# Performance work log

Measured on AMD Instinct MI355X. Metric: run time of the kernel, lower is better.

Reference implementation:

```python
import jax, jax.numpy as jnp
import numpy as np

SIGMA = 0.15
POS_W, ANG_W, WID_W, SCORE_W = 1.0, 1.0, 1.0, 0.5


def setup_inputs() -> dict:
    N, MAXC = 262144, 32
    rng = np.random.default_rng(0)
    counts = rng.integers(0, MAXC, size=N)
    M = int(counts.sum())
    key = jax.random.key(0)
    k1, k2, k3 = jax.random.split(key, 3)
    pred = jax.random.normal(k1, (N, 6), jnp.float32)
    gt = jax.random.normal(k2, (M, 6), jnp.float32)
    # GT score is a BCE target: keep it in [0, 1)
    gt = gt.at[:, 5].set(jax.random.uniform(k3, (M,), jnp.float32))
    return {
        "pred": pred,
        "all_gt_grasps": gt,
        "gt_counts": jnp.asarray(counts, jnp.int32),
    }


def reference(pred, all_gt_grasps, gt_counts):
    N = pred.shape[0]
    M = all_gt_grasps.shape[0]
    # CSR-style ragged layout: segment id of each GT row
    seg = jnp.repeat(jnp.arange(N), gt_counts, total_repeat_length=M)  # (M,)
    has_gt = gt_counts > 0                                             # (N,)

    # Step 1: squared distance from each GT to its prediction's center
    ppos = pred[seg, :2]                                               # (M,2)
    sq_dist = jnp.sum((ppos - all_gt_grasps[:, :2]) ** 2, axis=1)      # (M,)

    # Step 2: Gaussian tolerance position loss (per-segment max response)
    resp = jnp.exp(-sq_dist / (2.0 * SIGMA ** 2))
    max_resp = jax.ops.segment_max(resp, seg, num_segments=N)
    loss_pos = jnp.where(has_gt, 1.0 - max_resp, 0.0)

    # Step 3: nearest GT per prediction (first argmin, matching torch.argmin)
    seg_min = jax.ops.segment_min(sq_dist, seg, num_segments=N)
    cand = jnp.where(sq_dist == seg_min[seg], jnp.arange(M), M)
    nearest = jax.ops.segment_min(cand, seg, num_segments=N)
    nearest = jnp.where(has_gt, jnp.minimum(nearest, M - 1), 0)
    ng = all_gt_grasps[nearest]                                        # (N,6)

    # Step 4: angle (L1 on cos/sin), width (smooth L1), score (BCE-with-logits)
    loss_angle = jnp.where(
        has_gt,
        jnp.abs(pred[:, 2] - ng[:, 2]) + jnp.abs(pred[:, 3] - ng[:, 3]),
        0.0,
    )
    d = pred[:, 4] - ng[:, 4]
    ad = jnp.abs(d)
    smooth_l1 = jnp.where(ad < 1.0, 0.5 * d * d, ad - 0.5)
    loss_width = jnp.where(has_gt, smooth_l1, 0.0)

    x, t = pred[:, 5], ng[:, 5]
    bce = jnp.maximum(x, 0.0) - x * t + jnp.log1p(jnp.exp(-jnp.abs(x)))
    loss_score = jnp.where(has_gt & (t > 0), bce, 0.0)

    lp = loss_pos.mean()
    la = loss_angle.mean()
    lw = loss_width.mean()
    ls = loss_score.mean()
    lg = POS_W * lp + ANG_W * la + WID_W * lw + SCORE_W * ls
    return jnp.stack([lp, la, lw, ls, lg])
```

## Files before the change

kernel.cpp:

```cpp
#include <hip/hip_runtime.h>
#include <math.h>
#include <float.h>

#define BS 256
#define MAXC 31
typedef unsigned int u32;


__global__ void block_sum_kernel(const int* __restrict__ counts,
                                 int* __restrict__ blockSums, int N) {
    int i = blockIdx.x * BS + threadIdx.x;
    int v = (i < N) ? counts[i] : 0;
    for (int o = 32; o > 0; o >>= 1) v += __shfl_down(v, o, 64);
    __shared__ int ws[BS / 64];
    int lane = threadIdx.x & 63, w = threadIdx.x >> 6;
    if (lane == 0) ws[w] = v;
    __syncthreads();
    if (threadIdx.x == 0) {
        int s = 0;
        for (int ww = 0; ww < BS / 64; ++ww) s += ws[ww];
        blockSums[blockIdx.x] = s;
    }
}

__global__ void __launch_bounds__(BS)
fused_kernel(const float* __restrict__ pred, const float* __restrict__ gt,
             const int* __restrict__ counts, const int* __restrict__ blockSums,
             float4* __restrict__ partials, int N) {
    const int t = threadIdx.x;
    const int b = blockIdx.x;
    const int i = b * BS + t;
    const int lane = t & 63, w = t >> 6;

    __shared__ int waveTot[BS / 64];
    __shared__ int basePart[BS / 64];
    __shared__ float red[BS / 64][4];

    const int c = (i < N) ? counts[i] : 0;
    int incl = c;
    for (int o = 1; o < 64; o <<= 1) {
        int x = __shfl_up(incl, o, 64);
        if (lane >= o) incl += x;
    }
    if (lane == 63) waveTot[w] = incl;

    int acc = 0;
#pragma unroll
    for (int k = 0; k < 4; ++k) {
        const int idx = t + BS * k;
        if (idx < b) acc += blockSums[idx];
    }
    for (int o = 32; o > 0; o >>= 1) acc += __shfl_down(acc, o, 64);
    if (lane == 0) basePart[w] = acc;
    __syncthreads();

    int wbase = 0;
    for (int ww = 0; ww < w; ++ww) wbase += waveTot[ww];
    const int base = basePart[0] + basePart[1] + basePart[2] + basePart[3];
    const int gStart = base + wbase + incl - c;

    const float2* gxy = reinterpret_cast<const float2*>(gt);
    const float2 myp = (i < N)
        ? reinterpret_cast<const float2*>(pred)[(size_t)i * 3]
        : make_float2(0.f, 0.f);

    float best = FLT_MAX;
    int bestRow = 0;

#pragma unroll
    for (int j = 0; j < MAXC; ++j) {
        if (j < c) {
            const float2 g = gxy[(size_t)(gStart + j) * 3];
            const float dx = myp.x - g.x, dy = myp.y - g.y;
            const float d2 = dx * dx + dy * dy;
            if (d2 < best) { best = d2; bestRow = gStart + j; }
        }
    }

    float lp = 0.f, la = 0.f, lw = 0.f, ls = 0.f;
    if (i < N && c > 0) {
        lp = 1.0f - expf(-best / 0.045f);

        const float* p = pred + (size_t)i * 6;
        const float2 p23 = *reinterpret_cast<const float2*>(p + 2);
        const float2 p45 = *reinterpret_cast<const float2*>(p + 4);
        const float* ng = gt + (size_t)bestRow * 6;
        const float2 g23 = *reinterpret_cast<const float2*>(ng + 2);
        const float2 g45 = *reinterpret_cast<const float2*>(ng + 4);

        la = fabsf(p23.x - g23.x) + fabsf(p23.y - g23.y);
        const float d = p45.x - g45.x;
        const float ad = fabsf(d);
        lw = (ad < 1.0f) ? 0.5f * d * d : ad - 0.5f;
        const float x = p45.y;
        if (g45.y > 0.0f) {
            ls = fmaxf(x, 0.0f) - x * g45.y + log1pf(expf(-fabsf(x)));
        }
    }

    for (int o = 32; o > 0; o >>= 1) {
        lp += __shfl_down(lp, o, 64);
        la += __shfl_down(la, o, 64);
        lw += __shfl_down(lw, o, 64);
        ls += __shfl_down(ls, o, 64);
    }
    if (lane == 0) { red[w][0] = lp; red[w][1] = la; red[w][2] = lw; red[w][3] = ls; }
    __syncthreads();
    if (t == 0) {
        float s0 = 0, s1 = 0, s2 = 0, s3 = 0;
        for (int ww = 0; ww < BS / 64; ++ww) {
            s0 += red[ww][0]; s1 += red[ww][1]; s2 += red[ww][2]; s3 += red[ww][3];
        }
        partials[b] = make_float4(s0, s1, s2, s3);
    }
}

__global__ void finalize_kernel(const float4* __restrict__ partials,
                                float* __restrict__ out, int nb, int N) {
    const int t = threadIdx.x;
    const int lane = t & 63, w = t >> 6;
    double s0 = 0, s1 = 0, s2 = 0, s3 = 0;
    if (t < nb) {
        const float4 v = partials[t];
        s0 = v.x; s1 = v.y; s2 = v.z; s3 = v.w;
    }
    for (int o = 32; o > 0; o >>= 1) {
        s0 += __shfl_down(s0, o, 64);
        s1 += __shfl_down(s1, o, 64);
        s2 += __shfl_down(s2, o, 64);
        s3 += __shfl_down(s3, o, 64);
    }
    __shared__ double red[16][4];
    if (lane == 0) { red[w][0] = s0; red[w][1] = s1; red[w][2] = s2; red[w][3] = s3; }
    __syncthreads();
    if (t == 0) {
        double t0 = 0, t1 = 0, t2 = 0, t3 = 0;
        for (int ww = 0; ww < blockDim.x / 64; ++ww) {
            t0 += red[ww][0]; t1 += red[ww][1]; t2 += red[ww][2]; t3 += red[ww][3];
        }
        const double inv = 1.0 / (double)N;
        const float lp = (float)(t0 * inv);
        const float la = (float)(t1 * inv);
        const float lw = (float)(t2 * inv);
        const float ls = (float)(t3 * inv);
        out[0] = lp; out[1] = la; out[2] = lw; out[3] = ls;
        out[4] = lp + la + lw + 0.5f * ls;
    }
}

extern "C" void kernel_launch(void* const* d_in, const int* in_sizes, int n_in,
                              void* d_out, int out_size, void* d_ws, size_t ws_size,
                              hipStream_t stream) {
    const float* pred = (const float*)d_in[0];
    const float* gt = (const float*)d_in[1];
    const int* counts = (const int*)d_in[2];
    float* out = (float*)d_out;

    const int N = in_sizes[2];
    const int numBlocks = (N + BS - 1) / BS;

    int* blockSums = (int*)d_ws;
    float4* partials = (float4*)((char*)d_ws + 8192);

    block_sum_kernel<<<numBlocks, BS, 0, stream>>>(counts, blockSums, N);
    fused_kernel<<<numBlocks, BS, 0, stream>>>(pred, gt, counts, blockSums,
                                               partials, N);
    finalize_kernel<<<1, 1024, 0, stream>>>(partials, out, numBlocks, N);
}
```

Baseline: 179.7 us.

## Stage block's GT rows in shared memory via coalesced float4 loads

Each block now cooperatively copies its contiguous range of GT rows into LDS in chunks of 1536 rows, using coalesced float4 loads aligned via a pad row. Threads then scan their own segment from shared memory and keep the nearest GT's angle, width and score fields in registers, which removes the strided per-thread gathers and the second global load of the nearest row. The cost is about 36KB of LDS per block, which lowers occupancy, plus extra barriers and a chunk loop.

```diff
diff --git a/kernel.cpp b/kernel.cpp
--- a/kernel.cpp
+++ b/kernel.cpp
@@ -4,7 +4,9 @@
 
 #define BS 256
 #define MAXC 31
-typedef unsigned int u32;
+#define CH 1536
+#define CHF4 (CH * 24 / 16)
+#define LPT (CHF4 / BS)
 
 
 __global__ void block_sum_kernel(const int* __restrict__ counts,
@@ -32,8 +34,10 @@
     const int i = b * BS + t;
     const int lane = t & 63, w = t >> 6;
 
+    __shared__ float4 chunk4[CHF4 + 1];
     __shared__ int waveTot[BS / 64];
     __shared__ int basePart[BS / 64];
+    __shared__ int sTotal;
     __shared__ float red[BS / 64][4];
 
     const int c = (i < N) ? counts[i] : 0;
@@ -57,24 +61,61 @@
     int wbase = 0;
     for (int ww = 0; ww < w; ++ww) wbase += waveTot[ww];
     const int base = basePart[0] + basePart[1] + basePart[2] + basePart[3];
-    const int gStart = base + wbase + incl - c;
-
-    const float2* gxy = reinterpret_cast<const float2*>(gt);
+    const int myStart = wbase + incl - c;
+    const int myEnd = myStart + c;
+    if (t == BS - 1) sTotal = myEnd;
+    __syncthreads();
+
+    const int blockTotal = sTotal;
+    const int pad = base & 1;
+    const int totalRows = blockTotal + pad;
+    const size_t startByte = (size_t)(base - pad) * 24;
+    const float4* gt4 = reinterpret_cast<const float4*>(
+        reinterpret_cast<const char*>(gt) + startByte);
+    const float2* cf2 = reinterpret_cast<const float2*>(chunk4);
+
     const float2 myp = (i < N)
         ? reinterpret_cast<const float2*>(pred)[(size_t)i * 3]
         : make_float2(0.f, 0.f);
 
     float best = FLT_MAX;
-    int bestRow = 0;
-
+    float2 bg23 = make_float2(0.f, 0.f);
+    float2 bg45 = make_float2(0.f, 0.f);
+
+    for (int row0 = 0; row0 < totalRows; row0 += CH) {
+        const int rowsHere = min(CH, totalRows - row0);
+        const int bytesHere = rowsHere * 24;
+        const int nf4 = bytesHere >> 4;
+        const int f4Base = row0 * 3 / 2;
 #pragma unroll
-    for (int j = 0; j < MAXC; ++j) {
-        if (j < c) {
-            const float2 g = gxy[(size_t)(gStart + j) * 3];
+        for (int u = 0; u < LPT; ++u) {
+            const int idx = u * BS + t;
+            if (idx < nf4) chunk4[idx] = gt4[f4Base + idx];
+        }
+        if (t == 0 && (bytesHere & 15)) {
+            reinterpret_cast<float2*>(chunk4)[nf4 * 2] =
+                *reinterpret_cast<const float2*>(
+                    reinterpret_cast<const char*>(gt) + startByte +
+                    (size_t)row0 * 24 + (size_t)nf4 * 16);
+        }
+        __syncthreads();
+
+        const int cLo = row0 - pad;
+        const int cHi = cLo + rowsHere;
+        const int lo = myStart > cLo ? myStart : cLo;
+        const int hi = myEnd < cHi ? myEnd : cHi;
+        for (int j = lo; j < hi; ++j) {
+            const int rr = j + pad - row0;
+            const float2 g = cf2[rr * 3];
             const float dx = myp.x - g.x, dy = myp.y - g.y;
             const float d2 = dx * dx + dy * dy;
-            if (d2 < best) { best = d2; bestRow = gStart + j; }
-        }
+            if (d2 < best) {
+                best = d2;
+                bg23 = cf2[rr * 3 + 1];
+                bg45 = cf2[rr * 3 + 2];
+            }
+        }
+        if (row0 + CH < totalRows) __syncthreads();
     }
 
     float lp = 0.f, la = 0.f, lw = 0.f, ls = 0.f;
@@ -84,17 +125,14 @@
         const float* p = pred + (size_t)i * 6;
         const float2 p23 = *reinterpret_cast<const float2*>(p + 2);
         const float2 p45 = *reinterpret_cast<const float2*>(p + 4);
-        const float* ng = gt + (size_t)bestRow * 6;
-        const float2 g23 = *reinterpret_cast<const float2*>(ng + 2);
-        const float2 g45 = *reinterpret_cast<const float2*>(ng + 4);
-
-        la = fabsf(p23.x - g23.x) + fabsf(p23.y - g23.y);
-        const float d = p45.x - g45.x;
+
+        la = fabsf(p23.x - bg23.x) + fabsf(p23.y - bg23.y);
+        const float d = p45.x - bg45.x;
         const float ad = fabsf(d);
         lw = (ad < 1.0f) ? 0.5f * d * d : ad - 0.5f;
         const float x = p45.y;
-        if (g45.y > 0.0f) {
-            ls = fmaxf(x, 0.0f) - x * g45.y + log1pf(expf(-fabsf(x)));
+        if (bg45.y > 0.0f) {
+            ls = fmaxf(x, 0.0f) - x * bg45.y + log1pf(expf(-fabsf(x)));
         }
     }
 
```

After: 168.3 us. 6.3% less time.
